# Optimization experiments

Measured on AMD Instinct MI355X. Metric: run time of the kernel, lower is better.

Reference implementation:

```python
import jax, jax.numpy as jnp
import numpy as np

DN = ('NCHW', 'OIHW', 'NCHW')

def setup_inputs() -> dict:
    key = jax.random.key(0)
    ks = jax.random.split(key, 7)
    N, C_in, H, W = 32, 512, 56, 56
    C_sq, C_e1, C_e3 = 64, 256, 256
    def p(k, shape, fan_in):
        bound = 1.0 / np.sqrt(fan_in)
        return jax.random.uniform(k, shape, jnp.float32, -bound, bound)
    return {
        'x': jax.random.normal(ks[0], (N, C_in, H, W), jnp.float32),
        'w_sq': p(ks[1], (C_sq, C_in, 1, 1), C_in),
        'b_sq': p(ks[2], (C_sq,), C_in),
        'w_1x1': p(ks[3], (C_e1, C_sq, 1, 1), C_sq),
        'b_1x1': p(ks[4], (C_e1,), C_sq),
        'w_3x3': p(ks[5], (C_e3, C_sq, 3, 3), C_sq * 9),
        'b_3x3': p(ks[6], (C_e3,), C_sq * 9),
    }

def reference(x, w_sq, b_sq, w_1x1, b_1x1, w_3x3, b_3x3):
    # squeeze: 1x1 conv + ReLU
    s = jax.lax.conv_general_dilated(x, w_sq, (1, 1), 'VALID', dimension_numbers=DN)
    s = jax.nn.relu(s + b_sq[None, :, None, None])
    # expand 1x1 branch
    e1 = jax.lax.conv_general_dilated(s, w_1x1, (1, 1), 'VALID', dimension_numbers=DN)
    e1 = jax.nn.relu(e1 + b_1x1[None, :, None, None])
    # expand 3x3 branch, padding=1
    e3 = jax.lax.conv_general_dilated(s, w_3x3, (1, 1), ((1, 1), (1, 1)), dimension_numbers=DN)
    e3 = jax.nn.relu(e3 + b_3x3[None, :, None, None])
    return jnp.concatenate([e1, e3], axis=1)
```

## Files before the change

### kernel.cpp

```cpp
#include <hip/hip_runtime.h>
#include <hip/hip_bf16.h>
#include <stdint.h>

typedef __attribute__((ext_vector_type(8))) short bf16x8;
typedef __attribute__((ext_vector_type(4))) float f32x4;

#define GLB(p) ((const __attribute__((address_space(1))) void*)(p))
#define LDSP(p) ((__attribute__((address_space(3))) void*)(p))

#define HW    3136
#define WIMG  56
#define PROW  58
#define PNR   59
#define SIMG  (PNR * PROW)
#define C_IN  512

static __device__ __forceinline__ unsigned short f2bf(float f) {
    unsigned u = __builtin_bit_cast(unsigned, f);
    return (unsigned short)((u + 0x7FFFu + ((u >> 16) & 1u)) >> 16);
}

__global__ void zero_s(uint4* __restrict__ s) {
    const unsigned total = 32u * SIMG * 8;
    for (unsigned i = blockIdx.x * 256 + threadIdx.x; i < total; i += gridDim.x * 256) {
        uint4 z; z.x = z.y = z.z = z.w = 0;
        s[i] = z;
    }
}

__global__ void prep_weights(const float* __restrict__ wsq,
                             const float* __restrict__ w1,
                             const float* __restrict__ w3,
                             unsigned short* __restrict__ wsq_bf,
                             unsigned short* __restrict__ w1_bf,
                             unsigned short* __restrict__ w3r_bf) {
    int t = blockIdx.x * 256 + threadIdx.x;
    if (t < 32768) wsq_bf[t] = f2bf(wsq[t]);
    if (t < 16384) w1_bf[t] = f2bf(w1[t]);
    if (t < 147456) {
        int j = t >> 14;
        int rem = t & 16383;
        int o = rem >> 6, c = rem & 63;
        w3r_bf[t] = f2bf(w3[(o * 64 + c) * 9 + j]);
    }
}

__global__ __launch_bounds__(256, 4) void squeeze_kernel(
    const float* __restrict__ x, const float* __restrict__ b_sq,
    const unsigned short* __restrict__ wsq_bf, unsigned short* __restrict__ s)
{
    __shared__ uint8_t xs[2][8192];
    const int n = blockIdx.y, hw0 = blockIdx.x * 64;
    const int tid = threadIdx.x;
    const int w = tid >> 6, l = tid & 63, lx = l & 15, lk = l >> 4;

    const uint8_t* xbase = (const uint8_t*)(x + (size_t)n * C_IN * HW + hw0);

    auto stage = [&](int buf, int kb) {
        #pragma unroll
        for (int q = 0; q < 2; ++q) {
            int c = q * 256 + tid;
            int r = c >> 4, g = c & 15;
            const uint8_t* src = xbase + (size_t)(kb * 32 + r) * (HW * 4)
                                       + ((g * 16) ^ (((r >> 3) & 3) << 6));
            __builtin_amdgcn_global_load_lds(GLB(src), LDSP(&xs[buf][c * 16]), 16, 0, 0);
        }
    };

    stage(0, 0);
    __syncthreads();

    f32x4 acc[4] = {};
    const unsigned short* ap = wsq_bf + (16 * w + lx) * C_IN + lk * 8;
    const int swz = lk << 6;

    for (int kb = 0; kb < 16; ++kb) {
        const int cur = kb & 1;
        if (kb < 15) stage(cur ^ 1, kb + 1);
        bf16x8 a = *(const bf16x8*)(ap + kb * 32);
        #pragma unroll
        for (int nf = 0; nf < 4; ++nf) {
            const uint8_t* base = &xs[cur][lk * 2048 + (((nf * 16 + lx) * 4) ^ swz)];
            float f[8];
            #pragma unroll
            for (int i = 0; i < 8; ++i) f[i] = *(const float*)(base + i * 256);
            union { uint32_t u[4]; bf16x8 v; } bb;
            #pragma unroll
            for (int h = 0; h < 4; ++h)
                asm("v_cvt_pk_bf16_f32 %0, %1, %2" : "=v"(bb.u[h]) : "v"(f[2*h]), "v"(f[2*h+1]));
            acc[nf] = __builtin_amdgcn_mfma_f32_16x16x32_bf16(a, bb.v, acc[nf], 0, 0, 0);
        }
        __syncthreads();
    }

    const int c0 = 16 * w + lk * 4;
    float4 bias = *(const float4*)(b_sq + c0);
    const float* bp = (const float*)&bias;
    uint8_t* sn = (uint8_t*)s + (size_t)n * SIMG * 128;
    #pragma unroll
    for (int nf = 0; nf < 4; ++nf) {
        int col = hw0 + nf * 16 + lx;
        int p = col + 59 + 2 * (col / WIMG);
        unsigned short v[4];
        #pragma unroll
        for (int r = 0; r < 4; ++r) v[r] = f2bf(fmaxf(acc[nf][r] + bp[r], 0.0f));
        uint2 pk;
        pk.x = (unsigned)v[0] | ((unsigned)v[1] << 16);
        pk.y = (unsigned)v[2] | ((unsigned)v[3] << 16);
        *(uint2*)(sn + (size_t)p * 128 + ((c0 * 2) ^ ((p & 7) << 4))) = pk;
    }
}

__global__ __launch_bounds__(256, 4) void expand_kernel(
    const unsigned short* __restrict__ s,
    const unsigned short* __restrict__ w1_bf,
    const unsigned short* __restrict__ w3r_bf,
    const float* __restrict__ b1, const float* __restrict__ b3,
    float* __restrict__ out)
{
    __shared__ uint8_t tile[37120];
    const int n = blockIdx.z, mt = blockIdx.y, hw0 = blockIdx.x * 64;
    const int tid = threadIdx.x;
    const int w = tid >> 6, l = tid & 63, lx = l & 15, lk = l >> 4;
    const int y0 = hw0 / WIMG;

    const uint8_t* src = (const uint8_t*)s + ((size_t)n * SIMG + y0 * PROW) * 128;
    #pragma unroll
    for (int it = 0; it < 9; ++it) {
        int c = it * 256 + tid;
        __builtin_amdgcn_global_load_lds(GLB(src + (size_t)c * 16), LDSP(&tile[c * 16]), 16, 0, 0);
    }
    if (tid < 16)
        __builtin_amdgcn_global_load_lds(GLB(src + (size_t)(2304 + tid) * 16),
                                         LDSP(&tile[(2304 + tid) * 16]), 16, 0, 0);
    __syncthreads();

    int pg[4], tb[4];
    #pragma unroll
    for (int nf = 0; nf < 4; ++nf) {
        int hw = hw0 + nf * 16 + lx;
        int p = hw + 59 + 2 * (hw / WIMG);
        pg[nf] = p;
        tb[nf] = (p - y0 * PROW) * 128;
    }
    const int cb = 64 * mt + 16 * w;
    const int lk16 = lk * 16;
    float* outn = out + (size_t)n * 512 * HW;

    {
        f32x4 acc[4] = {};
        #pragma unroll
        for (int k0 = 0; k0 < 2; ++k0) {
            bf16x8 b = *(const bf16x8*)(w1_bf + (cb + lx) * 64 + k0 * 32 + lk * 8);
            #pragma unroll
            for (int nf = 0; nf < 4; ++nf) {
                int sw = (pg[nf] & 7) << 4;
                bf16x8 a = *(const bf16x8*)&tile[tb[nf] + ((lk16 + k0 * 64) ^ sw)];
                acc[nf] = __builtin_amdgcn_mfma_f32_16x16x32_bf16(a, b, acc[nf], 0, 0, 0);
            }
        }
        float bias = b1[cb + lx];
        float* op = outn + (size_t)(cb + lx) * HW + hw0 + lk * 4;
        #pragma unroll
        for (int nf = 0; nf < 4; ++nf) {
            float4 v;
            v.x = fmaxf(acc[nf][0] + bias, 0.0f);
            v.y = fmaxf(acc[nf][1] + bias, 0.0f);
            v.z = fmaxf(acc[nf][2] + bias, 0.0f);
            v.w = fmaxf(acc[nf][3] + bias, 0.0f);
            *(float4*)(op + nf * 16) = v;
        }
    }

    {
        f32x4 acc[4] = {};
        #pragma unroll
        for (int j = 0; j < 9; ++j) {
            const int doff = (j / 3 - 1) * PROW + (j % 3 - 1);
            const unsigned short* wj = w3r_bf + j * 16384 + (cb + lx) * 64;
            bf16x8 b0 = *(const bf16x8*)(wj + lk * 8);
            bf16x8 b1v = *(const bf16x8*)(wj + 32 + lk * 8);
            #pragma unroll
            for (int nf = 0; nf < 4; ++nf) {
                int pt = pg[nf] + doff;
                int sw = (pt & 7) << 4;
                int base = tb[nf] + doff * 128;
                bf16x8 a0 = *(const bf16x8*)&tile[base + (lk16 ^ sw)];
                acc[nf] = __builtin_amdgcn_mfma_f32_16x16x32_bf16(a0, b0, acc[nf], 0, 0, 0);
                bf16x8 a1 = *(const bf16x8*)&tile[base + ((lk16 + 64) ^ sw)];
                acc[nf] = __builtin_amdgcn_mfma_f32_16x16x32_bf16(a1, b1v, acc[nf], 0, 0, 0);
            }
        }
        float bias = b3[cb + lx];
        float* op = outn + (size_t)(256 + cb + lx) * HW + hw0 + lk * 4;
        #pragma unroll
        for (int nf = 0; nf < 4; ++nf) {
            float4 v;
            v.x = fmaxf(acc[nf][0] + bias, 0.0f);
            v.y = fmaxf(acc[nf][1] + bias, 0.0f);
            v.z = fmaxf(acc[nf][2] + bias, 0.0f);
            v.w = fmaxf(acc[nf][3] + bias, 0.0f);
            *(float4*)(op + nf * 16) = v;
        }
    }
}

extern "C" void kernel_launch(void* const* d_in, const int* in_sizes, int n_in,
                              void* d_out, int out_size, void* d_ws, size_t ws_size,
                              hipStream_t stream) {
    const float* x   = (const float*)d_in[0];
    const float* wsq = (const float*)d_in[1];
    const float* bsq = (const float*)d_in[2];
    const float* w1  = (const float*)d_in[3];
    const float* b1  = (const float*)d_in[4];
    const float* w3  = (const float*)d_in[5];
    const float* b3  = (const float*)d_in[6];
    float* out = (float*)d_out;

    unsigned short* wsq_bf = (unsigned short*)d_ws;
    unsigned short* w1_bf  = wsq_bf + 32768;
    unsigned short* w3r_bf = w1_bf + 16384;
    unsigned short* s      = w3r_bf + 147456;

    zero_s<<<1712, 256, 0, stream>>>((uint4*)s);
    prep_weights<<<576, 256, 0, stream>>>(wsq, w1, w3, wsq_bf, w1_bf, w3r_bf);
    squeeze_kernel<<<dim3(49, 32), 256, 0, stream>>>(x, bsq, wsq_bf, s);
    expand_kernel<<<dim3(49, 4, 32), 256, 0, stream>>>(s, w1_bf, w3r_bf, b1, b3, out);
}
```

Before: 429.3 us.

## Merge prep kernels, zero only halo, retile squeeze/expand warps, swizzle expand blocks

The zero and weight-prep kernels become one launch, and it zeroes only the padded border of the squeeze buffer instead of the whole buffer. The squeeze kernel gives each warp its own 16 columns across all 64 output channels, so each x element is converted from fp32 to bf16 once rather than once per warp. The expand kernel uses 2x2 warp tiles over channels and positions, which reuses the A and B fragments. It also remaps a flat grid so that neighbouring block IDs are spread across the 8 XCDs. The extra weight loads in squeeze and the changed output write pattern could offset some of the gain.

```diff
diff --git a/kernel.cpp b/kernel.cpp
--- a/kernel.cpp
+++ b/kernel.cpp
@@ -20,28 +20,32 @@
     return (unsigned short)((u + 0x7FFFu + ((u >> 16) & 1u)) >> 16);
 }
 
-__global__ void zero_s(uint4* __restrict__ s) {
-    const unsigned total = 32u * SIMG * 8;
-    for (unsigned i = blockIdx.x * 256 + threadIdx.x; i < total; i += gridDim.x * 256) {
-        uint4 z; z.x = z.y = z.z = z.w = 0;
-        s[i] = z;
-    }
-}
-
-__global__ void prep_weights(const float* __restrict__ wsq,
-                             const float* __restrict__ w1,
-                             const float* __restrict__ w3,
-                             unsigned short* __restrict__ wsq_bf,
-                             unsigned short* __restrict__ w1_bf,
-                             unsigned short* __restrict__ w3r_bf) {
-    int t = blockIdx.x * 256 + threadIdx.x;
-    if (t < 32768) wsq_bf[t] = f2bf(wsq[t]);
-    if (t < 16384) w1_bf[t] = f2bf(w1[t]);
-    if (t < 147456) {
-        int j = t >> 14;
-        int rem = t & 16383;
+__global__ void prep_kernel(const float* __restrict__ wsq,
+                            const float* __restrict__ w1,
+                            const float* __restrict__ w3,
+                            unsigned short* __restrict__ wsq_bf,
+                            unsigned short* __restrict__ w1_bf,
+                            unsigned short* __restrict__ w3r_bf,
+                            unsigned short* __restrict__ s) {
+    const int b = blockIdx.x, tid = threadIdx.x;
+    if (b < 576) {
+        int t = b * 256 + tid;
+        if (t < 32768) wsq_bf[t] = f2bf(wsq[t]);
+        if (t < 16384) w1_bf[t] = f2bf(w1[t]);
+        int j = t >> 14, rem = t & 16383;
         int o = rem >> 6, c = rem & 63;
         w3r_bf[t] = f2bf(w3[(o * 64 + c) * 9 + j]);
+    } else {
+        const int img = b - 576;
+        uint4* sn = (uint4*)(s + (size_t)img * SIMG * 64);
+        uint4 z; z.x = z.y = z.z = z.w = 0;
+        for (int t = tid; t < 1824; t += 256) {
+            int cell = t >> 3, q = t & 7;
+            int row, col;
+            if (cell < 116) { row = (cell >= 58) ? 57 : 0; col = cell % 58; }
+            else { int c2 = cell - 116; row = 1 + (c2 >> 1); col = (c2 & 1) * 57; }
+            sn[(size_t)(row * PROW + col) * 8 + q] = z;
+        }
     }
 }
 
@@ -71,43 +75,47 @@
     __syncthreads();
 
     f32x4 acc[4] = {};
-    const unsigned short* ap = wsq_bf + (16 * w + lx) * C_IN + lk * 8;
+    const unsigned short* ap = wsq_bf + lx * C_IN + lk * 8;
+    const int colb4 = ((w * 16 + lx) * 4);
     const int swz = lk << 6;
 
     for (int kb = 0; kb < 16; ++kb) {
         const int cur = kb & 1;
         if (kb < 15) stage(cur ^ 1, kb + 1);
-        bf16x8 a = *(const bf16x8*)(ap + kb * 32);
-        #pragma unroll
-        for (int nf = 0; nf < 4; ++nf) {
-            const uint8_t* base = &xs[cur][lk * 2048 + (((nf * 16 + lx) * 4) ^ swz)];
-            float f[8];
-            #pragma unroll
-            for (int i = 0; i < 8; ++i) f[i] = *(const float*)(base + i * 256);
-            union { uint32_t u[4]; bf16x8 v; } bb;
-            #pragma unroll
-            for (int h = 0; h < 4; ++h)
-                asm("v_cvt_pk_bf16_f32 %0, %1, %2" : "=v"(bb.u[h]) : "v"(f[2*h]), "v"(f[2*h+1]));
-            acc[nf] = __builtin_amdgcn_mfma_f32_16x16x32_bf16(a, bb.v, acc[nf], 0, 0, 0);
-        }
+        const uint8_t* bbase = &xs[cur][lk * 2048 + (colb4 ^ swz)];
+        float f[8];
+        #pragma unroll
+        for (int i = 0; i < 8; ++i) f[i] = *(const float*)(bbase + i * 256);
+        union { uint32_t u[4]; bf16x8 v; } bb;
+        #pragma unroll
+        for (int h = 0; h < 4; ++h)
+            asm("v_cvt_pk_bf16_f32 %0, %1, %2" : "=v"(bb.u[h]) : "v"(f[2*h]), "v"(f[2*h+1]));
+        bf16x8 a[4];
+        #pragma unroll
+        for (int mt = 0; mt < 4; ++mt)
+            a[mt] = *(const bf16x8*)(ap + mt * 16 * C_IN + kb * 32);
+        #pragma unroll
+        for (int mt = 0; mt < 4; ++mt)
+            acc[mt] = __builtin_amdgcn_mfma_f32_16x16x32_bf16(a[mt], bb.v, acc[mt], 0, 0, 0);
         __syncthreads();
     }
 
-    const int c0 = 16 * w + lk * 4;
-    float4 bias = *(const float4*)(b_sq + c0);
-    const float* bp = (const float*)&bias;
-    uint8_t* sn = (uint8_t*)s + (size_t)n * SIMG * 128;
+    const int col = hw0 + w * 16 + lx;
+    const int p = col + 59 + 2 * (col / WIMG);
+    uint8_t* sn = (uint8_t*)s + (size_t)n * SIMG * 128 + (size_t)p * 128;
+    const int psw = (p & 7) << 4;
     #pragma unroll
-    for (int nf = 0; nf < 4; ++nf) {
-        int col = hw0 + nf * 16 + lx;
-        int p = col + 59 + 2 * (col / WIMG);
+    for (int mt = 0; mt < 4; ++mt) {
+        const int c0 = mt * 16 + lk * 4;
+        float4 bias = *(const float4*)(b_sq + c0);
+        const float* bp = (const float*)&bias;
         unsigned short v[4];
         #pragma unroll
-        for (int r = 0; r < 4; ++r) v[r] = f2bf(fmaxf(acc[nf][r] + bp[r], 0.0f));
+        for (int r = 0; r < 4; ++r) v[r] = f2bf(fmaxf(acc[mt][r] + bp[r], 0.0f));
         uint2 pk;
         pk.x = (unsigned)v[0] | ((unsigned)v[1] << 16);
         pk.y = (unsigned)v[2] | ((unsigned)v[3] << 16);
-        *(uint2*)(sn + (size_t)p * 128 + ((c0 * 2) ^ ((p & 7) << 4))) = pk;
+        *(uint2*)(sn + ((c0 * 2) ^ psw)) = pk;
     }
 }
 
@@ -119,10 +127,17 @@
     float* __restrict__ out)
 {
     __shared__ uint8_t tile[37120];
-    const int n = blockIdx.z, mt = blockIdx.y, hw0 = blockIdx.x * 64;
+    const int bid = blockIdx.x;
+    const int ord = (bid & 7) * 784 + (bid >> 3);
+    const int n = ord / 196;
+    const int r2 = ord - n * 196;
+    const int mt = r2 / 49;
+    const int ht = r2 - mt * 49;
+    const int hw0 = ht * 64, y0 = hw0 / WIMG;
+
     const int tid = threadIdx.x;
     const int w = tid >> 6, l = tid & 63, lx = l & 15, lk = l >> 4;
-    const int y0 = hw0 / WIMG;
+    const int wm = w >> 1, wn = w & 1;
 
     const uint8_t* src = (const uint8_t*)s + ((size_t)n * SIMG + y0 * PROW) * 128;
     #pragma unroll
@@ -135,72 +150,90 @@
                                          LDSP(&tile[(2304 + tid) * 16]), 16, 0, 0);
     __syncthreads();
 
-    int pg[4], tb[4];
+    const int cb = mt * 64 + wm * 32;
+    const int hb = hw0 + wn * 32;
+    int pg[2], tb[2];
     #pragma unroll
-    for (int nf = 0; nf < 4; ++nf) {
-        int hw = hw0 + nf * 16 + lx;
+    for (int nf = 0; nf < 2; ++nf) {
+        int hw = hb + nf * 16 + lx;
         int p = hw + 59 + 2 * (hw / WIMG);
         pg[nf] = p;
         tb[nf] = (p - y0 * PROW) * 128;
     }
-    const int cb = 64 * mt + 16 * w;
     const int lk16 = lk * 16;
     float* outn = out + (size_t)n * 512 * HW;
 
     {
-        f32x4 acc[4] = {};
+        f32x4 acc[2][2] = {};
         #pragma unroll
         for (int k0 = 0; k0 < 2; ++k0) {
-            bf16x8 b = *(const bf16x8*)(w1_bf + (cb + lx) * 64 + k0 * 32 + lk * 8);
-            #pragma unroll
-            for (int nf = 0; nf < 4; ++nf) {
-                int sw = (pg[nf] & 7) << 4;
-                bf16x8 a = *(const bf16x8*)&tile[tb[nf] + ((lk16 + k0 * 64) ^ sw)];
-                acc[nf] = __builtin_amdgcn_mfma_f32_16x16x32_bf16(a, b, acc[nf], 0, 0, 0);
+            bf16x8 bw[2], av[2];
+            #pragma unroll
+            for (int bt = 0; bt < 2; ++bt)
+                bw[bt] = *(const bf16x8*)(w1_bf + (cb + bt * 16 + lx) * 64 + k0 * 32 + lk * 8);
+            #pragma unroll
+            for (int nf = 0; nf < 2; ++nf)
+                av[nf] = *(const bf16x8*)&tile[tb[nf] + ((lk16 + k0 * 64) ^ ((pg[nf] & 7) << 4))];
+            #pragma unroll
+            for (int bt = 0; bt < 2; ++bt)
+                #pragma unroll
+                for (int nf = 0; nf < 2; ++nf)
+                    acc[bt][nf] = __builtin_amdgcn_mfma_f32_16x16x32_bf16(av[nf], bw[bt], acc[bt][nf], 0, 0, 0);
+        }
+        #pragma unroll
+        for (int bt = 0; bt < 2; ++bt) {
+            float bias = b1[cb + bt * 16 + lx];
+            float* op = outn + (size_t)(cb + bt * 16 + lx) * HW + hb + lk * 4;
+            #pragma unroll
+            for (int nf = 0; nf < 2; ++nf) {
+                float4 v;
+                v.x = fmaxf(acc[bt][nf][0] + bias, 0.0f);
+                v.y = fmaxf(acc[bt][nf][1] + bias, 0.0f);
+                v.z = fmaxf(acc[bt][nf][2] + bias, 0.0f);
+                v.w = fmaxf(acc[bt][nf][3] + bias, 0.0f);
+                *(float4*)(op + nf * 16) = v;
             }
         }
-        float bias = b1[cb + lx];
-        float* op = outn + (size_t)(cb + lx) * HW + hw0 + lk * 4;
-        #pragma unroll
-        for (int nf = 0; nf < 4; ++nf) {
-            float4 v;
-            v.x = fmaxf(acc[nf][0] + bias, 0.0f);
-            v.y = fmaxf(acc[nf][1] + bias, 0.0f);
-            v.z = fmaxf(acc[nf][2] + bias, 0.0f);
-            v.w = fmaxf(acc[nf][3] + bias, 0.0f);
-            *(float4*)(op + nf * 16) = v;
-        }
     }
 
     {
-        f32x4 acc[4] = {};
+        f32x4 acc[2][2] = {};
         #pragma unroll
         for (int j = 0; j < 9; ++j) {
             const int doff = (j / 3 - 1) * PROW + (j % 3 - 1);
-            const unsigned short* wj = w3r_bf + j * 16384 + (cb + lx) * 64;
-            bf16x8 b0 = *(const bf16x8*)(wj + lk * 8);
-            bf16x8 b1v = *(const bf16x8*)(wj + 32 + lk * 8);
-            #pragma unroll
-            for (int nf = 0; nf < 4; ++nf) {
-                int pt = pg[nf] + doff;
-                int sw = (pt & 7) << 4;
-                int base = tb[nf] + doff * 128;
-                bf16x8 a0 = *(const bf16x8*)&tile[base + (lk16 ^ sw)];
-                acc[nf] = __builtin_amdgcn_mfma_f32_16x16x32_bf16(a0, b0, acc[nf], 0, 0, 0);
-                bf16x8 a1 = *(const bf16x8*)&tile[base + ((lk16 + 64) ^ sw)];
-                acc[nf] = __builtin_amdgcn_mfma_f32_16x16x32_bf16(a1, b1v, acc[nf], 0, 0, 0);
+            const unsigned short* wj = w3r_bf + j * 16384;
+            #pragma unroll
+            for (int k0 = 0; k0 < 2; ++k0) {
+                bf16x8 bw[2], av[2];
+                #pragma unroll
+                for (int bt = 0; bt < 2; ++bt)
+                    bw[bt] = *(const bf16x8*)(wj + (cb + bt * 16 + lx) * 64 + k0 * 32 + lk * 8);
+                #pragma unroll
+                for (int nf = 0; nf < 2; ++nf) {
+                    int pt = pg[nf] + doff;
+                    av[nf] = *(const bf16x8*)&tile[tb[nf] + doff * 128 +
+                                                  ((lk16 + k0 * 64) ^ ((pt & 7) << 4))];
+                }
+                #pragma unroll
+                for (int bt = 0; bt < 2; ++bt)
+                    #pragma unroll
+                    for (int nf = 0; nf < 2; ++nf)
+                        acc[bt][nf] = __builtin_amdgcn_mfma_f32_16x16x32_bf16(av[nf], bw[bt], acc[bt][nf], 0, 0, 0);
             }
         }
-        float bias = b3[cb + lx];
-        float* op = outn + (size_t)(256 + cb + lx) * HW + hw0 + lk * 4;
-        #pragma unroll
-        for (int nf = 0; nf < 4; ++nf) {
-            float4 v;
-            v.x = fmaxf(acc[nf][0] + bias, 0.0f);
-            v.y = fmaxf(acc[nf][1] + bias, 0.0f);
-            v.z = fmaxf(acc[nf][2] + bias, 0.0f);
-            v.w = fmaxf(acc[nf][3] + bias, 0.0f);
-            *(float4*)(op + nf * 16) = v;
+        #pragma unroll
+        for (int bt = 0; bt < 2; ++bt) {
+            float bias = b3[cb + bt * 16 + lx];
+            float* op = outn + (size_t)(256 + cb + bt * 16 + lx) * HW + hb + lk * 4;
+            #pragma unroll
+            for (int nf = 0; nf < 2; ++nf) {
+                float4 v;
+                v.x = fmaxf(acc[bt][nf][0] + bias, 0.0f);
+                v.y = fmaxf(acc[bt][nf][1] + bias, 0.0f);
+                v.z = fmaxf(acc[bt][nf][2] + bias, 0.0f);
+                v.w = fmaxf(acc[bt][nf][3] + bias, 0.0f);
+                *(float4*)(op + nf * 16) = v;
+            }
         }
     }
 }
@@ -222,8 +255,7 @@
     unsigned short* w3r_bf = w1_bf + 16384;
     unsigned short* s      = w3r_bf + 147456;
 
-    zero_s<<<1712, 256, 0, stream>>>((uint4*)s);
-    prep_weights<<<576, 256, 0, stream>>>(wsq, w1, w3, wsq_bf, w1_bf, w3r_bf);
+    prep_kernel<<<608, 256, 0, stream>>>(wsq, w1, w3, wsq_bf, w1_bf, w3r_bf, s);
     squeeze_kernel<<<dim3(49, 32), 256, 0, stream>>>(x, bsq, wsq_bf, s);
-    expand_kernel<<<dim3(49, 4, 32), 256, 0, stream>>>(s, w1_bf, w3r_bf, b1, b3, out);
-}
+    expand_kernel<<<6272, 256, 0, stream>>>(s, w1_bf, w3r_bf, b1, b3, out);
+}
```

Measured after the change: 467.8 us. 9.0% more time.
